# Kernel tuning notes

Hardware: AMD Instinct MI355X
Metric: run time of the kernel (lower is better)

The kernel has to match this reference:

```python
import jax, jax.numpy as jnp
import numpy as np

B, N, H, D = 64, 197, 10, 64  # batch, tokens (14x14 patches + cls), heads, head_dim
MAX_REL = 14
TABLE_ROWS = 2 * MAX_REL + 2  # 30


def _rel_indices(n, max_rel):
    """2D relative-position index matrices (AutoFormer RelativePosition2D_super)."""
    s = int(np.sqrt(n))  # patch grid side (14)
    r = np.arange(n)
    dist_v = r[None, :] // s - r[:, None] // s  # row distance
    dist_h = r[None, :] % s - r[:, None] % s   # col distance
    iv = np.clip(dist_v, -max_rel, max_rel) + max_rel + 1
    ih = np.clip(dist_h, -max_rel, max_rel) + max_rel + 1
    # cls token row/col get index 0
    iv = np.pad(iv[1:, 1:], ((1, 0), (1, 0)), constant_values=0)
    ih = np.pad(ih[1:, 1:], ((1, 0), (1, 0)), constant_values=0)
    return jnp.asarray(iv, jnp.int32), jnp.asarray(ih, jnp.int32)


_IV, _IH = _rel_indices(N, MAX_REL)


def setup_inputs() -> dict:
    key = jax.random.key(0)
    ks = jax.random.split(key, 5)
    return {
        "x": jax.random.normal(ks[0], (B, N, 3 * H * D), dtype=jnp.float32),
        "k_table_v": jax.random.normal(ks[1], (TABLE_ROWS, D), dtype=jnp.float32) * 0.02,
        "k_table_h": jax.random.normal(ks[2], (TABLE_ROWS, D), dtype=jnp.float32) * 0.02,
        "v_table_v": jax.random.normal(ks[3], (TABLE_ROWS, D), dtype=jnp.float32) * 0.02,
        "v_table_h": jax.random.normal(ks[4], (TABLE_ROWS, D), dtype=jnp.float32) * 0.02,
    }


def reference(x, k_table_v, k_table_h, v_table_v, v_table_h):
    scale = D ** (-0.5)
    # relative position embeddings: [N, N, D]
    rel_k = k_table_v[_IV] + k_table_h[_IH]
    rel_v = v_table_v[_IV] + v_table_h[_IH]
    # fused qkv -> q, k, v each [B, H, N, D]
    qkv = x.reshape(B, N, 3, H, D).transpose(2, 0, 3, 1, 4)
    q, k, v = qkv[0], qkv[1], qkv[2]
    # content scores + query/relative-key bias, fused before one softmax
    attn = (jnp.einsum('bhid,bhjd->bhij', q, k)
            + jnp.einsum('bhid,ijd->bhij', q, rel_k)) * scale
    attn = jax.nn.softmax(attn, axis=-1)
    # attn_drop has p=0 -> identity
    # value path + attn/relative-value bias, output laid out [B, N, H, D]
    out = (jnp.einsum('bhij,bhjd->bihd', attn, v)
           + jnp.einsum('bhij,ijd->bihd', attn, rel_v))
    # head_choice == max_heads -> final F.pad is a no-op
    return out.reshape(B, N, H * D)
```

## Files before the change

kernel.cpp:

```cpp
#include <hip/hip_runtime.h>
#include <hip/hip_bf16.h>

#define NTOK 197
#define NHEAD 10
#define XROW 1920

typedef __attribute__((ext_vector_type(8))) short short8;
typedef __attribute__((ext_vector_type(4))) float f32x4;

union S8U { short8 v; unsigned short u[8]; };

__device__ __forceinline__ unsigned short f2b(float f) {
    union { float f; unsigned int i; } a; a.f = f;
    unsigned int r = a.i + 0x7FFFu + ((a.i >> 16) & 1u);
    return (unsigned short)(r >> 16);
}

__device__ __forceinline__ short8 cvt8(const float* p) {
    const float4* s4 = (const float4*)p;
    float4 f0 = s4[0], f1 = s4[1];
    S8U t;
    t.u[0] = f2b(f0.x); t.u[1] = f2b(f0.y); t.u[2] = f2b(f0.z); t.u[3] = f2b(f0.w);
    t.u[4] = f2b(f1.x); t.u[5] = f2b(f1.y); t.u[6] = f2b(f1.z); t.u[7] = f2b(f1.w);
    return t.v;
}

#define OFF_K   0
#define OFF_IND 26624
#define OFF_VT  39936
#define OFF_T   72704
#define OFF_BM  80896
#define OFF_P   97280
#define LDS_TOTAL 162816

#define MFMA(a, b, c) __builtin_amdgcn_mfma_f32_16x16x32_bf16(a, b, c, 0, 0, 0)

__global__ __launch_bounds__(512)
void attn_super(const float* __restrict__ x,
                const float* __restrict__ ktv, const float* __restrict__ kth,
                const float* __restrict__ vtv, const float* __restrict__ vth,
                float* __restrict__ out)
{
    extern __shared__ char smem[];
    char* const Ks   = smem + OFF_K;
    char* const Inds = smem + OFF_IND;
    char* const VT   = smem + OFF_VT;
    char* const Ts   = smem + OFF_T;
    char* const Bms  = smem + OFF_BM;
    char* const Pr   = smem + OFF_P;

    const int tid = threadIdx.x;
    const int bb = blockIdx.x / NHEAD;
    const int hh = blockIdx.x - bb * NHEAD;
    const float* const xq = x + (size_t)bb * NTOK * XROW + hh * 64;

    #pragma unroll
    for (int it = 0; it < 4; ++it) {
        int cid = tid + it * 512;
        if (cid < 1664) {
            int row = cid >> 3, cc = cid & 7;
            S8U t;
            #pragma unroll
            for (int e = 0; e < 8; ++e) t.u[e] = 0;
            if (row < NTOK) t.v = cvt8(xq + 640 + (size_t)row * XROW + cc * 8);
            *(short8*)(Ks + row * 128 + ((cc ^ (row & 7)) * 16)) = t.v;
        }
    }
    #pragma unroll
    for (int it = 0; it < 2; ++it) {
        int cid = tid + it * 512;
        if (cid < 832) {
            int row = cid >> 2, c4 = cid & 3;
            S8U t;
            #pragma unroll
            for (int e = 0; e < 8; ++e) {
                int c = c4 * 8 + e;
                int on = 0;
                if (row < NTOK) {
                    if (c <= 14)      on = (row >= 1) && (row / 14 == c);
                    else if (c <= 28) on = (row >= 1) && (row % 14 == c - 15);
                    else if (c == 29) on = (row == 0);
                }
                t.u[e] = on ? 0x3F80 : 0;
            }
            *(short8*)(Inds + row * 64 + c4 * 16) = t.v;
        }
    }
    {
        int d = tid & 63, grp = tid >> 6;
        #pragma unroll
        for (int it = 0; it < 4; ++it) {
            int jc = grp + it * 8;
            if (jc < 25) {
                int j0 = jc * 8;
                S8U t;
                #pragma unroll
                for (int e = 0; e < 8; ++e) {
                    int j = j0 + e;
                    t.u[e] = (j < NTOK) ? f2b(xq[1280 + (size_t)j * XROW + d]) : (unsigned short)0;
                }
                *(short8*)(VT + d * 512 + ((jc ^ (d & 7)) * 16)) = t.v;
            }
        }
        #pragma unroll
        for (int it = 0; it < 8; ++it) {
            int r = grp + it * 8;
            if (r < 59) {
                float v;
                if (r == 0)       v = vtv[d] + vth[d];
                else if (r <= 29) v = vtv[r * 64 + d];
                else              v = vth[(r - 29) * 64 + d];
                int slot = 197 + r;
                int ch = (slot >> 3) ^ (d & 7);
                *(unsigned short*)(VT + d * 512 + ch * 16 + (slot & 7) * 2) = f2b(v);
            }
        }
    }
    {
        int row = tid >> 3, cc = tid & 7;
        S8U t;
        #pragma unroll
        for (int e = 0; e < 8; ++e) {
            float v = 0.f;
            int dc = cc * 8 + e;
            if (row <= 29)      v = ktv[row * 64 + dc];
            else if (row <= 59) v = kth[(row - 30) * 64 + dc];
            else if (row == 60) v = ktv[dc] + kth[dc];
            t.u[e] = f2b(v);
        }
        *(short8*)(Ts + row * 128 + ((cc ^ (row & 7)) * 16)) = t.v;
    }
    #pragma unroll
    for (int it = 0; it < 2; ++it) {
        int cid = tid + it * 512;
        int row = cid >> 5, cc = cid & 31;
        S8U t;
        #pragma unroll
        for (int e = 0; e < 8; ++e) {
            int j = cc * 8 + e;
            int on = 0;
            if (j < NTOK) {
                if (row <= 14)      on = (j >= 1) && (j / 14 == row);
                else if (row == 15) on = (j == 0);
                else if (row <= 29) on = (j >= 1) && (j % 14 == row - 16);
            }
            t.u[e] = on ? 0x3F80 : 0;
        }
        *(short8*)(Bms + row * 512 + ((cc ^ (row & 7)) * 16)) = t.v;
    }
    __syncthreads();

    const int w  = tid >> 6, l = tid & 63;
    const int lm = l & 15,  lg = l >> 4;
    const f32x4 fzero = {0.f, 0.f, 0.f, 0.f};
    char* const Pw  = Pr + w * 8192;
    char* const Aug = Pw;

    for (int rt = w; rt < 13; rt += 8) {
        int qrow = rt * 16 + lm;
        const float* qp = xq + (size_t)qrow * XROW;
        short8 afq[2];
        #pragma unroll
        for (int s = 0; s < 2; ++s) {
            S8U t;
            #pragma unroll
            for (int e = 0; e < 8; ++e) t.u[e] = 0;
            if (qrow < NTOK) t.v = cvt8(qp + (s * 4 + lg) * 8);
            afq[s] = t.v;
        }
        f32x4 qd[4];
        #pragma unroll
        for (int n = 0; n < 4; ++n) qd[n] = fzero;
        #pragma unroll
        for (int s = 0; s < 2; ++s) {
            #pragma unroll
            for (int n = 0; n < 4; ++n) {
                int tr = n * 16 + lm;
                short8 tf = *(const short8*)(Ts + tr * 128 + (((s * 4 + lg) ^ (tr & 7)) * 16));
                qd[n] = MFMA(afq[s], tf, qd[n]);
            }
        }
        *(short8*)(Aug + l * 16) = short8{0,0,0,0,0,0,0,0};
        #pragma unroll
        for (int n = 0; n < 4; ++n) {
            int r = n * 16 + lm;
            #pragma unroll
            for (int reg = 0; reg < 4; ++reg) {
                int i = rt * 16 + lg * 4 + reg;
                if (i == 0 || i >= NTOK) continue;
                int col = -1;
                if (r <= 29)      { int c = r - 15 + i / 14; if (c >= 0 && c <= 14) col = c; }
                else if (r <= 59) { int c = r - 45 + i % 14; if (c >= 0 && c <= 13) col = 15 + c; }
                else if (r == 60) col = 29;
                if (col >= 0) {
                    int row = lg * 4 + reg;
                    *(unsigned short*)(Aug + row * 64 + (((col >> 3) ^ (row & 3)) * 16)
                                       + (col & 7) * 2) = f2b(qd[n][reg]);
                }
            }
        }
        if (rt == 0 && l == 12) {
            unsigned short v = f2b(qd[3][0]);
            #pragma unroll
            for (int c = 0; c <= 14; ++c) *(unsigned short*)(Aug + c * 2) = v;
            *(unsigned short*)(Aug + 29 * 2) = v;
        }
        short8 af2 = *(const short8*)(Aug + lm * 64 + ((lg ^ (lm & 3)) * 16));

        f32x4 acc[13];
        #pragma unroll
        for (int ct = 0; ct < 13; ++ct) acc[ct] = fzero;
        #pragma unroll
        for (int ct = 0; ct < 13; ++ct) {
            int r = ct * 16 + lm;
            short8 bf0 = *(const short8*)(Ks + r * 128 + ((lg ^ (r & 7)) * 16));
            acc[ct] = MFMA(afq[0], bf0, acc[ct]);
            short8 bf1 = *(const short8*)(Ks + r * 128 + (((4 + lg) ^ (r & 7)) * 16));
            acc[ct] = MFMA(afq[1], bf1, acc[ct]);
            short8 bfi = *(const short8*)(Inds + r * 64 + lg * 16);
            acc[ct] = MFMA(af2, bfi, acc[ct]);
        }
        #pragma unroll
        for (int ct = 0; ct < 13; ++ct) {
            acc[ct][0] *= 0.125f; acc[ct][1] *= 0.125f;
            acc[ct][2] *= 0.125f; acc[ct][3] *= 0.125f;
        }
        if (lm >= 5) {
            acc[12][0] = -INFINITY; acc[12][1] = -INFINITY;
            acc[12][2] = -INFINITY; acc[12][3] = -INFINITY;
        }
        #pragma unroll
        for (int reg = 0; reg < 4; ++reg) {
            float m = acc[0][reg];
            #pragma unroll
            for (int ct = 1; ct < 13; ++ct) m = fmaxf(m, acc[ct][reg]);
            m = fmaxf(m, __shfl_xor(m, 1)); m = fmaxf(m, __shfl_xor(m, 2));
            m = fmaxf(m, __shfl_xor(m, 4)); m = fmaxf(m, __shfl_xor(m, 8));
            float ss = 0.f;
            #pragma unroll
            for (int ct = 0; ct < 13; ++ct) {
                float p = __expf(acc[ct][reg] - m);
                acc[ct][reg] = p; ss += p;
            }
            ss += __shfl_xor(ss, 1); ss += __shfl_xor(ss, 2);
            ss += __shfl_xor(ss, 4); ss += __shfl_xor(ss, 8);
            float inv = 1.0f / ss;
            #pragma unroll
            for (int ct = 0; ct < 13; ++ct) acc[ct][reg] *= inv;
        }
        #pragma unroll
        for (int ct = 0; ct < 13; ++ct) {
            int colc = ct * 16 + lm;
            #pragma unroll
            for (int reg = 0; reg < 4; ++reg) {
                int row = lg * 4 + reg;
                *(unsigned short*)(Pw + row * 512 + (((colc >> 3) ^ (row & 7)) * 16)
                                   + (colc & 7) * 2) = f2b(acc[ct][reg]);
            }
        }
        #pragma unroll
        for (int zz = 0; zz < 2; ++zz) {
            int z = l + zz * 64;
            if (z < 96) {
                int row = z / 6, ch = 26 + (z - row * 6);
                *(short8*)(Pw + row * 512 + ((ch ^ (row & 7)) * 16)) = short8{0,0,0,0,0,0,0,0};
            }
        }
        f32x4 bc[2]; bc[0] = fzero; bc[1] = fzero;
        #pragma unroll
        for (int s = 0; s < 7; ++s) {
            short8 pf = *(const short8*)(Pw + lm * 512 + (((s * 4 + lg) ^ (lm & 7)) * 16));
            #pragma unroll
            for (int n = 0; n < 2; ++n) {
                int tr = n * 16 + lm;
                short8 bmf = *(const short8*)(Bms + tr * 512 + (((s * 4 + lg) ^ (tr & 7)) * 16));
                bc[n] = MFMA(pf, bmf, bc[n]);
            }
        }
        #pragma unroll
        for (int n = 0; n < 2; ++n) {
            int t = n * 16 + lm;
            #pragma unroll
            for (int reg = 0; reg < 4; ++reg) {
                int row = lg * 4 + reg;
                int i = rt * 16 + row;
                if (i == 0) {
                    if (t == 15)
                        *(unsigned short*)(Pw + (24 * 16) + (197 & 7) * 2) = 0x3F80;
                    continue;
                }
                if (i >= NTOK) continue;
                int slot = -1;
                if (t <= 14)      slot = 197 + (t + 15 - i / 14);
                else if (t == 15) slot = 197;
                else if (t <= 29) slot = 226 + ((t - 16) + 15 - i % 14);
                if (slot >= 0)
                    *(unsigned short*)(Pw + row * 512 + (((slot >> 3) ^ (row & 7)) * 16)
                                       + (slot & 7) * 2) = f2b(bc[n][reg]);
            }
        }
        f32x4 o[4];
        #pragma unroll
        for (int nv = 0; nv < 4; ++nv) o[nv] = fzero;
        #pragma unroll
        for (int s = 0; s < 8; ++s) {
            short8 pf = *(const short8*)(Pw + lm * 512 + (((s * 4 + lg) ^ (lm & 7)) * 16));
            #pragma unroll
            for (int nv = 0; nv < 4; ++nv) {
                int vr = nv * 16 + lm;
                short8 vf = *(const short8*)(VT + vr * 512 + (((s * 4 + lg) ^ (vr & 7)) * 16));
                o[nv] = MFMA(pf, vf, o[nv]);
            }
        }
        #pragma unroll
        for (int reg = 0; reg < 4; ++reg) {
            int i = rt * 16 + lg * 4 + reg;
            if (i < NTOK) {
                float* dst = out + (size_t)bb * (NTOK * 640) + (size_t)i * 640 + hh * 64 + lm;
                #pragma unroll
                for (int nv = 0; nv < 4; ++nv) dst[nv * 16] = o[nv][reg];
            }
        }
    }
}

extern "C" void kernel_launch(void* const* d_in, const int* in_sizes, int n_in,
                              void* d_out, int out_size, void* d_ws, size_t ws_size,
                              hipStream_t stream) {
    const float* x   = (const float*)d_in[0];
    const float* ktv = (const float*)d_in[1];
    const float* kth = (const float*)d_in[2];
    const float* vtv = (const float*)d_in[3];
    const float* vth = (const float*)d_in[4];
    float* out = (float*)d_out;
    (void)hipFuncSetAttribute((const void*)attn_super,
                              hipFuncAttributeMaxDynamicSharedMemorySize, LDS_TOTAL);
    attn_super<<<dim3(64 * NHEAD), dim3(512), LDS_TOTAL, stream>>>(x, ktv, kth, vtv, vth, out);
}
```

Before: 214.0 us.

## Use 1024-thread blocks with one wave per query tile and transposed score MFMAs

The block grows to 1024 threads so each of the 13 query row tiles gets its own wave, removing the two-pass loop in which 5 of 8 waves handled a second tile. The QK MFMA operands are swapped so each lane holds a full score row, which turns the softmax reductions into two cross-lane shuffles and lets the probabilities be packed in registers and reused as MFMA A-fragments. The relative-value table moves into its own small LDS buffer, used by a separate two-step MFMA, so P no longer needs to be padded to 256 columns. K-table fragments are now read straight from global memory instead of being staged in LDS. The risks are three idle waves per block, and 1024-thread blocks with large LDS limiting occupancy to one block per CU.

Result: no change. 211.2 us (-1.3%).

```diff
diff --git a/kernel.cpp b/kernel.cpp
--- a/kernel.cpp
+++ b/kernel.cpp
@@ -8,7 +8,7 @@
 typedef __attribute__((ext_vector_type(8))) short short8;
 typedef __attribute__((ext_vector_type(4))) float f32x4;
 
-union S8U { short8 v; unsigned short u[8]; };
+union S8U { short8 v; unsigned short u[8]; unsigned int w[4]; };
 
 __device__ __forceinline__ unsigned short f2b(float f) {
     union { float f; unsigned int i; } a; a.f = f;
@@ -25,29 +25,29 @@
     return t.v;
 }
 
-#define OFF_K   0
-#define OFF_IND 26624
-#define OFF_VT  39936
-#define OFF_T   72704
-#define OFF_BM  80896
-#define OFF_P   97280
+#define OFF_K    0
+#define OFF_IND  26624
+#define OFF_VT   39936
+#define OFF_VTAB 72704
+#define OFF_BM   80896
+#define OFF_SCR  97280
 #define LDS_TOTAL 162816
 
 #define MFMA(a, b, c) __builtin_amdgcn_mfma_f32_16x16x32_bf16(a, b, c, 0, 0, 0)
 
-__global__ __launch_bounds__(512)
+__global__ __launch_bounds__(1024)
 void attn_super(const float* __restrict__ x,
                 const float* __restrict__ ktv, const float* __restrict__ kth,
                 const float* __restrict__ vtv, const float* __restrict__ vth,
                 float* __restrict__ out)
 {
     extern __shared__ char smem[];
-    char* const Ks   = smem + OFF_K;
-    char* const Inds = smem + OFF_IND;
-    char* const VT   = smem + OFF_VT;
-    char* const Ts   = smem + OFF_T;
-    char* const Bms  = smem + OFF_BM;
-    char* const Pr   = smem + OFF_P;
+    char* const Ks    = smem + OFF_K;
+    char* const Inds  = smem + OFF_IND;
+    char* const VT    = smem + OFF_VT;
+    char* const Vtab  = smem + OFF_VTAB;
+    char* const Bms   = smem + OFF_BM;
+    char* const Scr   = smem + OFF_SCR;
 
     const int tid = threadIdx.x;
     const int bb = blockIdx.x / NHEAD;
@@ -55,8 +55,8 @@
     const float* const xq = x + (size_t)bb * NTOK * XROW + hh * 64;
 
     #pragma unroll
-    for (int it = 0; it < 4; ++it) {
-        int cid = tid + it * 512;
+    for (int it = 0; it < 2; ++it) {
+        int cid = tid + it * 1024;
         if (cid < 1664) {
             int row = cid >> 3, cc = cid & 7;
             S8U t;
@@ -66,31 +66,27 @@
             *(short8*)(Ks + row * 128 + ((cc ^ (row & 7)) * 16)) = t.v;
         }
     }
-    #pragma unroll
-    for (int it = 0; it < 2; ++it) {
-        int cid = tid + it * 512;
-        if (cid < 832) {
-            int row = cid >> 2, c4 = cid & 3;
-            S8U t;
-            #pragma unroll
-            for (int e = 0; e < 8; ++e) {
-                int c = c4 * 8 + e;
-                int on = 0;
-                if (row < NTOK) {
-                    if (c <= 14)      on = (row >= 1) && (row / 14 == c);
-                    else if (c <= 28) on = (row >= 1) && (row % 14 == c - 15);
-                    else if (c == 29) on = (row == 0);
-                }
-                t.u[e] = on ? 0x3F80 : 0;
-            }
-            *(short8*)(Inds + row * 64 + c4 * 16) = t.v;
-        }
+    if (tid < 832) {
+        int row = tid >> 2, c4 = tid & 3;
+        S8U t;
+        #pragma unroll
+        for (int e = 0; e < 8; ++e) {
+            int c = c4 * 8 + e;
+            int on = 0;
+            if (row < NTOK) {
+                if (c <= 14)      on = (row >= 1) && (row / 14 == c);
+                else if (c <= 28) on = (row >= 1) && (row % 14 == c - 15);
+                else if (c == 29) on = (row == 0);
+            }
+            t.u[e] = on ? 0x3F80 : 0;
+        }
+        *(short8*)(Inds + row * 64 + ((c4 ^ (row & 3)) * 16)) = t.v;
     }
     {
         int d = tid & 63, grp = tid >> 6;
         #pragma unroll
-        for (int it = 0; it < 4; ++it) {
-            int jc = grp + it * 8;
+        for (int it = 0; it < 2; ++it) {
+            int jc = grp + it * 16;
             if (jc < 25) {
                 int j0 = jc * 8;
                 S8U t;
@@ -103,37 +99,18 @@
             }
         }
         #pragma unroll
-        for (int it = 0; it < 8; ++it) {
-            int r = grp + it * 8;
-            if (r < 59) {
-                float v;
-                if (r == 0)       v = vtv[d] + vth[d];
-                else if (r <= 29) v = vtv[r * 64 + d];
-                else              v = vth[(r - 29) * 64 + d];
-                int slot = 197 + r;
-                int ch = (slot >> 3) ^ (d & 7);
-                *(unsigned short*)(VT + d * 512 + ch * 16 + (slot & 7) * 2) = f2b(v);
-            }
+        for (int it = 0; it < 4; ++it) {
+            int r = grp + it * 16;
+            float v = 0.f;
+            if (r <= 29)      v = vtv[r * 64 + d];
+            else if (r <= 58) v = vth[(r - 29) * 64 + d];
+            else if (r == 59) v = vtv[d] + vth[d];
+            *(unsigned short*)(Vtab + d * 128 + (((r >> 3) ^ (d & 7)) * 16)
+                               + (r & 7) * 2) = f2b(v);
         }
     }
     {
-        int row = tid >> 3, cc = tid & 7;
-        S8U t;
-        #pragma unroll
-        for (int e = 0; e < 8; ++e) {
-            float v = 0.f;
-            int dc = cc * 8 + e;
-            if (row <= 29)      v = ktv[row * 64 + dc];
-            else if (row <= 59) v = kth[(row - 30) * 64 + dc];
-            else if (row == 60) v = ktv[dc] + kth[dc];
-            t.u[e] = f2b(v);
-        }
-        *(short8*)(Ts + row * 128 + ((cc ^ (row & 7)) * 16)) = t.v;
-    }
-    #pragma unroll
-    for (int it = 0; it < 2; ++it) {
-        int cid = tid + it * 512;
-        int row = cid >> 5, cc = cid & 31;
+        int row = tid >> 5, cc = tid & 31;
         S8U t;
         #pragma unroll
         for (int e = 0; e < 8; ++e) {
@@ -150,176 +127,216 @@
     }
     __syncthreads();
 
-    const int w  = tid >> 6, l = tid & 63;
-    const int lm = l & 15,  lg = l >> 4;
+    const int w = tid >> 6;
+    if (w >= 13) return;
+    const int rt = w;
+    const int l = tid & 63, lm = l & 15, lg = l >> 4;
     const f32x4 fzero = {0.f, 0.f, 0.f, 0.f};
-    char* const Pw  = Pr + w * 8192;
-    char* const Aug = Pw;
-
-    for (int rt = w; rt < 13; rt += 8) {
-        int qrow = rt * 16 + lm;
-        const float* qp = xq + (size_t)qrow * XROW;
-        short8 afq[2];
-        #pragma unroll
-        for (int s = 0; s < 2; ++s) {
+    char* const ScrW = Scr + w * 4096;
+
+    const int qrow = rt * 16 + lm;
+    const float* qp = xq + (size_t)qrow * XROW;
+    short8 afq[2];
+    #pragma unroll
+    for (int s = 0; s < 2; ++s) {
+        S8U t;
+        #pragma unroll
+        for (int e = 0; e < 8; ++e) t.u[e] = 0;
+        if (qrow < NTOK) t.v = cvt8(qp + (s * 4 + lg) * 8);
+        afq[s] = t.v;
+    }
+
+    f32x4 qd[4];
+    #pragma unroll
+    for (int n = 0; n < 4; ++n) qd[n] = fzero;
+    #pragma unroll
+    for (int s = 0; s < 2; ++s) {
+        int k0 = s * 32 + lg * 8;
+        #pragma unroll
+        for (int n = 0; n < 4; ++n) {
+            int tr = n * 16 + lm;
             S8U t;
-            #pragma unroll
-            for (int e = 0; e < 8; ++e) t.u[e] = 0;
-            if (qrow < NTOK) t.v = cvt8(qp + (s * 4 + lg) * 8);
-            afq[s] = t.v;
-        }
-        f32x4 qd[4];
-        #pragma unroll
-        for (int n = 0; n < 4; ++n) qd[n] = fzero;
-        #pragma unroll
-        for (int s = 0; s < 2; ++s) {
-            #pragma unroll
-            for (int n = 0; n < 4; ++n) {
-                int tr = n * 16 + lm;
-                short8 tf = *(const short8*)(Ts + tr * 128 + (((s * 4 + lg) ^ (tr & 7)) * 16));
-                qd[n] = MFMA(afq[s], tf, qd[n]);
-            }
-        }
-        *(short8*)(Aug + l * 16) = short8{0,0,0,0,0,0,0,0};
-        #pragma unroll
-        for (int n = 0; n < 4; ++n) {
-            int r = n * 16 + lm;
-            #pragma unroll
-            for (int reg = 0; reg < 4; ++reg) {
-                int i = rt * 16 + lg * 4 + reg;
-                if (i == 0 || i >= NTOK) continue;
-                int col = -1;
-                if (r <= 29)      { int c = r - 15 + i / 14; if (c >= 0 && c <= 14) col = c; }
-                else if (r <= 59) { int c = r - 45 + i % 14; if (c >= 0 && c <= 13) col = 15 + c; }
-                else if (r == 60) col = 29;
-                if (col >= 0) {
-                    int row = lg * 4 + reg;
-                    *(unsigned short*)(Aug + row * 64 + (((col >> 3) ^ (row & 3)) * 16)
-                                       + (col & 7) * 2) = f2b(qd[n][reg]);
-                }
-            }
-        }
-        if (rt == 0 && l == 12) {
-            unsigned short v = f2b(qd[3][0]);
-            #pragma unroll
-            for (int c = 0; c <= 14; ++c) *(unsigned short*)(Aug + c * 2) = v;
-            *(unsigned short*)(Aug + 29 * 2) = v;
-        }
-        short8 af2 = *(const short8*)(Aug + lm * 64 + ((lg ^ (lm & 3)) * 16));
-
-        f32x4 acc[13];
-        #pragma unroll
-        for (int ct = 0; ct < 13; ++ct) acc[ct] = fzero;
-        #pragma unroll
-        for (int ct = 0; ct < 13; ++ct) {
-            int r = ct * 16 + lm;
-            short8 bf0 = *(const short8*)(Ks + r * 128 + ((lg ^ (r & 7)) * 16));
-            acc[ct] = MFMA(afq[0], bf0, acc[ct]);
-            short8 bf1 = *(const short8*)(Ks + r * 128 + (((4 + lg) ^ (r & 7)) * 16));
-            acc[ct] = MFMA(afq[1], bf1, acc[ct]);
-            short8 bfi = *(const short8*)(Inds + r * 64 + lg * 16);
-            acc[ct] = MFMA(af2, bfi, acc[ct]);
-        }
-        #pragma unroll
-        for (int ct = 0; ct < 13; ++ct) {
-            acc[ct][0] *= 0.125f; acc[ct][1] *= 0.125f;
-            acc[ct][2] *= 0.125f; acc[ct][3] *= 0.125f;
-        }
-        if (lm >= 5) {
-            acc[12][0] = -INFINITY; acc[12][1] = -INFINITY;
-            acc[12][2] = -INFINITY; acc[12][3] = -INFINITY;
-        }
-        #pragma unroll
-        for (int reg = 0; reg < 4; ++reg) {
-            float m = acc[0][reg];
-            #pragma unroll
-            for (int ct = 1; ct < 13; ++ct) m = fmaxf(m, acc[ct][reg]);
-            m = fmaxf(m, __shfl_xor(m, 1)); m = fmaxf(m, __shfl_xor(m, 2));
-            m = fmaxf(m, __shfl_xor(m, 4)); m = fmaxf(m, __shfl_xor(m, 8));
-            float ss = 0.f;
-            #pragma unroll
-            for (int ct = 0; ct < 13; ++ct) {
-                float p = __expf(acc[ct][reg] - m);
-                acc[ct][reg] = p; ss += p;
-            }
-            ss += __shfl_xor(ss, 1); ss += __shfl_xor(ss, 2);
-            ss += __shfl_xor(ss, 4); ss += __shfl_xor(ss, 8);
-            float inv = 1.0f / ss;
-            #pragma unroll
-            for (int ct = 0; ct < 13; ++ct) acc[ct][reg] *= inv;
-        }
-        #pragma unroll
-        for (int ct = 0; ct < 13; ++ct) {
-            int colc = ct * 16 + lm;
-            #pragma unroll
-            for (int reg = 0; reg < 4; ++reg) {
-                int row = lg * 4 + reg;
-                *(unsigned short*)(Pw + row * 512 + (((colc >> 3) ^ (row & 7)) * 16)
-                                   + (colc & 7) * 2) = f2b(acc[ct][reg]);
-            }
-        }
-        #pragma unroll
-        for (int zz = 0; zz < 2; ++zz) {
-            int z = l + zz * 64;
-            if (z < 96) {
-                int row = z / 6, ch = 26 + (z - row * 6);
-                *(short8*)(Pw + row * 512 + ((ch ^ (row & 7)) * 16)) = short8{0,0,0,0,0,0,0,0};
-            }
-        }
-        f32x4 bc[2]; bc[0] = fzero; bc[1] = fzero;
-        #pragma unroll
-        for (int s = 0; s < 7; ++s) {
-            short8 pf = *(const short8*)(Pw + lm * 512 + (((s * 4 + lg) ^ (lm & 7)) * 16));
-            #pragma unroll
-            for (int n = 0; n < 2; ++n) {
-                int tr = n * 16 + lm;
-                short8 bmf = *(const short8*)(Bms + tr * 512 + (((s * 4 + lg) ^ (tr & 7)) * 16));
-                bc[n] = MFMA(pf, bmf, bc[n]);
-            }
-        }
-        #pragma unroll
-        for (int n = 0; n < 2; ++n) {
-            int t = n * 16 + lm;
-            #pragma unroll
-            for (int reg = 0; reg < 4; ++reg) {
-                int row = lg * 4 + reg;
-                int i = rt * 16 + row;
-                if (i == 0) {
-                    if (t == 15)
-                        *(unsigned short*)(Pw + (24 * 16) + (197 & 7) * 2) = 0x3F80;
-                    continue;
-                }
-                if (i >= NTOK) continue;
-                int slot = -1;
-                if (t <= 14)      slot = 197 + (t + 15 - i / 14);
-                else if (t == 15) slot = 197;
-                else if (t <= 29) slot = 226 + ((t - 16) + 15 - i % 14);
-                if (slot >= 0)
-                    *(unsigned short*)(Pw + row * 512 + (((slot >> 3) ^ (row & 7)) * 16)
-                                       + (slot & 7) * 2) = f2b(bc[n][reg]);
-            }
-        }
-        f32x4 o[4];
-        #pragma unroll
-        for (int nv = 0; nv < 4; ++nv) o[nv] = fzero;
-        #pragma unroll
-        for (int s = 0; s < 8; ++s) {
-            short8 pf = *(const short8*)(Pw + lm * 512 + (((s * 4 + lg) ^ (lm & 7)) * 16));
-            #pragma unroll
-            for (int nv = 0; nv < 4; ++nv) {
-                int vr = nv * 16 + lm;
-                short8 vf = *(const short8*)(VT + vr * 512 + (((s * 4 + lg) ^ (vr & 7)) * 16));
-                o[nv] = MFMA(pf, vf, o[nv]);
-            }
-        }
+            if (tr >= 61) {
+                #pragma unroll
+                for (int e = 0; e < 8; ++e) t.u[e] = 0;
+            } else if (tr == 60) {
+                #pragma unroll
+                for (int e = 0; e < 8; ++e) t.u[e] = f2b(ktv[k0 + e] + kth[k0 + e]);
+            } else {
+                const float* tp = (tr <= 29) ? (ktv + tr * 64) : (kth + (tr - 30) * 64);
+                t.v = cvt8(tp + k0);
+            }
+            qd[n] = MFMA(afq[s], t.v, qd[n]);
+        }
+    }
+
+    *(short8*)(ScrW + l * 16) = short8{0,0,0,0,0,0,0,0};
+    #pragma unroll
+    for (int n = 0; n < 4; ++n) {
+        int r = n * 16 + lm;
         #pragma unroll
         for (int reg = 0; reg < 4; ++reg) {
             int i = rt * 16 + lg * 4 + reg;
-            if (i < NTOK) {
-                float* dst = out + (size_t)bb * (NTOK * 640) + (size_t)i * 640 + hh * 64 + lm;
-                #pragma unroll
-                for (int nv = 0; nv < 4; ++nv) dst[nv * 16] = o[nv][reg];
-            }
+            if (i == 0 || i >= NTOK) continue;
+            int col = -1;
+            if (r <= 29)      { int c = r - 15 + i / 14; if (c >= 0 && c <= 14) col = c; }
+            else if (r <= 59) { int c = r - 45 + i % 14; if (c >= 0 && c <= 13) col = 15 + c; }
+            else if (r == 60) col = 29;
+            if (col >= 0) {
+                int row = lg * 4 + reg;
+                *(unsigned short*)(ScrW + row * 64 + (((col >> 3) ^ (row & 3)) * 16)
+                                   + (col & 7) * 2) = f2b(qd[n][reg]);
+            }
+        }
+    }
+    if (rt == 0 && l == 12) {
+        unsigned short v = f2b(qd[3][0]);
+        #pragma unroll
+        for (int c = 0; c <= 14; ++c) *(unsigned short*)(ScrW + c * 2) = v;
+        *(unsigned short*)(ScrW + 29 * 2) = v;
+    }
+    short8 af2 = *(const short8*)(ScrW + lm * 64 + ((lg ^ (lm & 3)) * 16));
+
+    f32x4 acc[13];
+    #pragma unroll
+    for (int ct = 0; ct < 13; ++ct) acc[ct] = fzero;
+    #pragma unroll
+    for (int ct = 0; ct < 13; ++ct) {
+        int jr = ct * 16 + lm;
+        short8 bf0 = *(const short8*)(Ks + jr * 128 + ((lg ^ (jr & 7)) * 16));
+        acc[ct] = MFMA(bf0, afq[0], acc[ct]);
+        short8 bf1 = *(const short8*)(Ks + jr * 128 + (((4 + lg) ^ (jr & 7)) * 16));
+        acc[ct] = MFMA(bf1, afq[1], acc[ct]);
+        short8 bfi = *(const short8*)(Inds + jr * 64 + ((lg ^ (jr & 3)) * 16));
+        acc[ct] = MFMA(bfi, af2, acc[ct]);
+    }
+
+    #pragma unroll
+    for (int ct = 0; ct < 13; ++ct) {
+        acc[ct][0] *= 0.125f; acc[ct][1] *= 0.125f;
+        acc[ct][2] *= 0.125f; acc[ct][3] *= 0.125f;
+    }
+    #pragma unroll
+    for (int reg = 0; reg < 4; ++reg)
+        if (lg * 4 + reg >= 5) acc[12][reg] = -INFINITY;
+    float m = -INFINITY;
+    #pragma unroll
+    for (int ct = 0; ct < 13; ++ct) {
+        m = fmaxf(m, fmaxf(fmaxf(acc[ct][0], acc[ct][1]), fmaxf(acc[ct][2], acc[ct][3])));
+    }
+    m = fmaxf(m, __shfl_xor(m, 16)); m = fmaxf(m, __shfl_xor(m, 32));
+    float ss = 0.f;
+    #pragma unroll
+    for (int ct = 0; ct < 13; ++ct) {
+        #pragma unroll
+        for (int reg = 0; reg < 4; ++reg) {
+            float p = __expf(acc[ct][reg] - m);
+            acc[ct][reg] = p; ss += p;
+        }
+    }
+    ss += __shfl_xor(ss, 16); ss += __shfl_xor(ss, 32);
+    float inv = 1.0f / ss;
+
+    unsigned int pp[13][2];
+    #pragma unroll
+    for (int ct = 0; ct < 13; ++ct) {
+        pp[ct][0] = (unsigned int)f2b(acc[ct][0] * inv) |
+                    ((unsigned int)f2b(acc[ct][1] * inv) << 16);
+        pp[ct][1] = (unsigned int)f2b(acc[ct][2] * inv) |
+                    ((unsigned int)f2b(acc[ct][3] * inv) << 16);
+    }
+
+    short8 af_p[7];
+    #pragma unroll
+    for (int ct = 0; ct < 8; ++ct) {
+        int ch = ct * 2 + (lg >> 1);
+        char* a = ScrW + lm * 256 + ((ch ^ (lm & 7)) * 16) + (lg & 1) * 8;
+        ((unsigned int*)a)[0] = pp[ct][0]; ((unsigned int*)a)[1] = pp[ct][1];
+    }
+    #pragma unroll
+    for (int s = 0; s < 4; ++s)
+        af_p[s] = *(const short8*)(ScrW + lm * 256 + (((s * 4 + lg) ^ (lm & 7)) * 16));
+    #pragma unroll
+    for (int ct = 8; ct < 13; ++ct) {
+        int ch = (ct - 8) * 2 + (lg >> 1);
+        char* a = ScrW + lm * 256 + ((ch ^ (lm & 7)) * 16) + (lg & 1) * 8;
+        ((unsigned int*)a)[0] = pp[ct][0]; ((unsigned int*)a)[1] = pp[ct][1];
+    }
+    if (lg < 2)
+        *(short8*)(ScrW + lm * 256 + (((10 + lg) ^ (lm & 7)) * 16)) = short8{0,0,0,0,0,0,0,0};
+    #pragma unroll
+    for (int s = 4; s < 7; ++s)
+        af_p[s] = *(const short8*)(ScrW + lm * 256 + ((((s - 4) * 4 + lg) ^ (lm & 7)) * 16));
+
+    f32x4 bc[2]; bc[0] = fzero; bc[1] = fzero;
+    #pragma unroll
+    for (int s = 0; s < 7; ++s) {
+        #pragma unroll
+        for (int n = 0; n < 2; ++n) {
+            int tr = n * 16 + lm;
+            short8 bmf = *(const short8*)(Bms + tr * 512 + (((s * 4 + lg) ^ (tr & 7)) * 16));
+            bc[n] = MFMA(af_p[s], bmf, bc[n]);
+        }
+    }
+
+    *(short8*)(ScrW + l * 32) = short8{0,0,0,0,0,0,0,0};
+    *(short8*)(ScrW + l * 32 + 16) = short8{0,0,0,0,0,0,0,0};
+    #pragma unroll
+    for (int n = 0; n < 2; ++n) {
+        int t = n * 16 + lm;
+        #pragma unroll
+        for (int reg = 0; reg < 4; ++reg) {
+            int row = lg * 4 + reg;
+            int i = rt * 16 + row;
+            if (i == 0) {
+                if (t == 15)
+                    *(unsigned short*)(ScrW + (((59 >> 3) ^ 0) * 16) + (59 & 7) * 2) = 0x3F80;
+                continue;
+            }
+            if (i >= NTOK) continue;
+            int col = -1;
+            if (t <= 14)      col = t + 15 - i / 14;
+            else if (t == 15) col = 59;
+            else              col = 29 + (t - 16) + 15 - i % 14;
+            if (col >= 0)
+                *(unsigned short*)(ScrW + row * 128 + (((col >> 3) ^ (row & 7)) * 16)
+                                   + (col & 7) * 2) = f2b(bc[n][reg]);
+        }
+    }
+    short8 ag[2];
+    #pragma unroll
+    for (int s = 0; s < 2; ++s)
+        ag[s] = *(const short8*)(ScrW + lm * 128 + (((s * 4 + lg) ^ (lm & 7)) * 16));
+
+    f32x4 o[4];
+    #pragma unroll
+    for (int nv = 0; nv < 4; ++nv) o[nv] = fzero;
+    #pragma unroll
+    for (int s = 0; s < 7; ++s) {
+        #pragma unroll
+        for (int nv = 0; nv < 4; ++nv) {
+            int d = nv * 16 + lm;
+            short8 vf = *(const short8*)(VT + d * 512 + (((s * 4 + lg) ^ (d & 7)) * 16));
+            o[nv] = MFMA(af_p[s], vf, o[nv]);
+        }
+    }
+    #pragma unroll
+    for (int s = 0; s < 2; ++s) {
+        #pragma unroll
+        for (int nv = 0; nv < 4; ++nv) {
+            int d = nv * 16 + lm;
+            short8 vtf = *(const short8*)(Vtab + d * 128 + (((s * 4 + lg) ^ (d & 7)) * 16));
+            o[nv] = MFMA(ag[s], vtf, o[nv]);
+        }
+    }
+
+    #pragma unroll
+    for (int reg = 0; reg < 4; ++reg) {
+        int i = rt * 16 + lg * 4 + reg;
+        if (i < NTOK) {
+            float* dst = out + (size_t)bb * (NTOK * 640) + (size_t)i * 640 + hh * 64 + lm;
+            #pragma unroll
+            for (int nv = 0; nv < 4; ++nv) dst[nv * 16] = o[nv][reg];
         }
     }
 }
@@ -335,5 +352,5 @@
     float* out = (float*)d_out;
     (void)hipFuncSetAttribute((const void*)attn_super,
                               hipFuncAttributeMaxDynamicSharedMemorySize, LDS_TOTAL);
-    attn_super<<<dim3(64 * NHEAD), dim3(512), LDS_TOTAL, stream>>>(x, ktv, kth, vtv, vth, out);
+    attn_super<<<dim3(64 * NHEAD), dim3(1024), LDS_TOTAL, stream>>>(x, ktv, kth, vtv, vth, out);
 }
```
